# Kernel optimization log

Measured on AMD Instinct MI355X. Metric: run time of the kernel, lower is better.

## Reference

```python
import jax, jax.numpy as jnp
import numpy as np
from jax.scipy.linalg import expm

D = 512      # d_model
S = 3        # num_scales
BATCH = 256
H = 8        # attention heads
HD = D // H  # head dim


def layernorm(x, g, b, eps=1e-5):
    m = jnp.mean(x, axis=-1, keepdims=True)
    v = jnp.var(x, axis=-1, keepdims=True)
    return (x - m) / jnp.sqrt(v + eps) * g + b


def setup_inputs() -> dict:
    key = jax.random.key(0)
    ks = jax.random.split(key, 16)
    sd = 1.0 / np.sqrt(D)
    inp = {
        'x': jax.random.normal(ks[0], (BATCH, D), jnp.float32),
        'h_prev': jax.random.normal(ks[1], (BATCH, D), jnp.float32),
        'lstm_h': jax.random.normal(ks[2], (S, BATCH, D), jnp.float32) * 0.1,
        'lstm_c': jax.random.normal(ks[3], (S, BATCH, D), jnp.float32) * 0.1,
        'A': jax.random.normal(ks[4], (D, D), jnp.float32) * sd,
        'Bm': jax.random.normal(ks[5], (D, D), jnp.float32) * sd,
        'dn_w1': jax.random.normal(ks[6], (D, D), jnp.float32) * sd,
        'dn_b1': jnp.zeros((D,), jnp.float32),
        'dn_g': jnp.ones((D,), jnp.float32),
        'dn_beta': jnp.zeros((D,), jnp.float32),
        'dn_w2': jax.random.normal(ks[7], (1, D), jnp.float32) * sd,
        'dn_b2': jnp.zeros((1,), jnp.float32),
        'lstm_wih': jax.random.normal(ks[8], (S, 4 * D, D), jnp.float32) * sd,
        'lstm_whh': jax.random.normal(ks[9], (S, 4 * D, D), jnp.float32) * sd,
        'lstm_bih': jnp.zeros((S, 4 * D), jnp.float32),
        'lstm_bhh': jnp.zeros((S, 4 * D), jnp.float32),
        'decays': jnp.linspace(0.5, 0.95, S, dtype=jnp.float32),
        'attn_in_w': jax.random.normal(ks[10], (3 * D, D), jnp.float32) * sd,
        'attn_in_b': jnp.zeros((3 * D,), jnp.float32),
        'attn_out_w': jax.random.normal(ks[11], (D, D), jnp.float32) * sd,
        'attn_out_b': jnp.zeros((D,), jnp.float32),
        'proj_w': jax.random.normal(ks[12], (D, (S + 2) * D), jnp.float32) * (1.0 / np.sqrt((S + 2) * D)),
        'proj_b': jnp.zeros((D,), jnp.float32),
        'proj_g': jnp.ones((D,), jnp.float32),
        'proj_beta': jnp.zeros((D,), jnp.float32),
    }
    return inp


def reference(x, h_prev, lstm_h, lstm_c, A, Bm, dn_w1, dn_b1, dn_g, dn_beta,
              dn_w2, dn_b2, lstm_wih, lstm_whh, lstm_bih, lstm_bhh, decays,
              attn_in_w, attn_in_b, attn_out_w, attn_out_b,
              proj_w, proj_b, proj_g, proj_beta):
    # ---- delta_net: Linear -> LayerNorm -> GELU(exact) -> Linear -> Softplus ----
    h1 = layernorm(x @ dn_w1.T + dn_b1, dn_g, dn_beta)
    h1 = jax.nn.gelu(h1, approximate=False)
    delta = jax.nn.softplus(h1 @ dn_w2.T + dn_b2)           # (B, 1)

    # ---- SSM update: h_t = expm(delta*A) h_prev + delta*B x ----
    A_disc = jax.vmap(expm)(delta[:, :, None] * A)          # (B, D, D)
    h_ssm = jnp.einsum('bij,bj->bi', A_disc, h_prev) + delta * jnp.einsum('ij,bj->bi', Bm, x)

    # ---- multi-scale LSTM cells (vectorized over scales) ----
    gates = (jnp.einsum('bd,skd->sbk', x, lstm_wih)
             + jnp.einsum('sbd,skd->sbk', lstm_h, lstm_whh)
             + (lstm_bih + lstm_bhh)[:, None, :])           # (S, B, 4D)
    gi, gf, gg, go = jnp.split(gates, 4, axis=-1)
    i_g = jax.nn.sigmoid(gi)
    f_g = jax.nn.sigmoid(gf)
    g_g = jnp.tanh(gg)
    o_g = jax.nn.sigmoid(go)
    c_raw = f_g * lstm_c + i_g * g_g                        # (S, B, D)
    h_new = o_g * jnp.tanh(c_raw)                           # (S, B, D)
    dec = decays[:, None, None]
    c_new = dec * lstm_c + (1.0 - dec) * c_raw              # (S, B, D)

    # ---- fusion attention: 1 query (h_ssm), S keys/values (h_new) ----
    Wq, Wk, Wv = jnp.split(attn_in_w, 3, axis=0)
    bq, bk, bv = jnp.split(attn_in_b, 3, axis=0)
    kv = jnp.transpose(h_new, (1, 0, 2))                    # (B, S, D)
    q = (h_ssm @ Wq.T + bq).reshape(-1, 1, H, HD).transpose(0, 2, 1, 3)   # (B,H,1,HD)
    k = (kv @ Wk.T + bk).reshape(-1, S, H, HD).transpose(0, 2, 1, 3)      # (B,H,S,HD)
    v = (kv @ Wv.T + bv).reshape(-1, S, H, HD).transpose(0, 2, 1, 3)
    scores = jnp.einsum('bhqe,bhke->bhqk', q, k) / np.sqrt(HD)
    attn = jax.nn.softmax(scores, axis=-1)
    ctx = jnp.einsum('bhqk,bhke->bhqe', attn, v)            # (B,H,1,HD)
    ctx = ctx.transpose(0, 2, 1, 3).reshape(-1, D)          # (B, D)
    fused = ctx @ attn_out_w.T + attn_out_b                 # (B, D)

    # ---- output projection over concat [h_ssm, fused, h_1..h_S] ----
    combined = jnp.concatenate([h_ssm, fused] + [h_new[i] for i in range(S)], axis=-1)
    output = layernorm(combined @ proj_w.T + proj_b, proj_g, proj_beta)
    return (output, h_ssm, h_new, c_new)
```

## Files before the change

kernel.cpp:

```cpp
#include <hip/hip_runtime.h>
#include <math.h>

#define DIM 512
#define NB 256
#define KMAX 12

using bf16x8 = __attribute__((ext_vector_type(8))) short;
using f32x4  = __attribute__((ext_vector_type(4))) float;
using float4v = __attribute__((ext_vector_type(4))) float;
using ushort4v = __attribute__((ext_vector_type(4))) unsigned short;

__device__ __forceinline__ unsigned short f2b(float f) {
    union { float f; unsigned int u; } v; v.f = f;
    unsigned int r = v.u + 0x7fffu + ((v.u >> 16) & 1u);
    return (unsigned short)(r >> 16);
}
__device__ __forceinline__ float b2f(unsigned short u) {
    union { unsigned int u; float f; } v; v.u = ((unsigned int)u) << 16;
    return v.f;
}
__device__ __forceinline__ ushort4v f2b4(float4v v) {
    ushort4v o;
    o.x = f2b(v.x); o.y = f2b(v.y); o.z = f2b(v.z); o.w = f2b(v.w);
    return o;
}

__device__ __forceinline__ void block_reduce2(float& s, float& q, float* sb1, float* sb2)
{
    int tid = threadIdx.x;
    #pragma unroll
    for (int off = 32; off > 0; off >>= 1) {
        s += __shfl_down(s, off);
        q += __shfl_down(q, off);
    }
    if ((tid & 63) == 0) { sb1[tid >> 6] = s; sb2[tid >> 6] = q; }
    __syncthreads();
    s = sb1[0] + sb1[1] + sb1[2] + sb1[3];
    q = sb2[0] + sb2[1] + sb2[2] + sb2[3];
    __syncthreads();
}

struct GemmDesc {
    const unsigned short* X;
    const unsigned short* W;
    const float* bias;
    float* Cf;
    unsigned short* Cb;
    unsigned short* Ct;
    int M, N, K, ldX, ldW, ldC, tr_row0, acc, xf32, wf32;
};
struct GemmArgs { GemmDesc d[10]; };
struct LnParams {
    const float* pre; const float* g; const float* beta;
    const float* w2; const float* b2; float* delta; float* coeff;
    int lnd_y;
};
struct PwParams {
    const float* gates; const float* bih; const float* bhh; const float* cin;
    const float* decays; float* hout; float* cout; unsigned short* combb;
    int pw_y;
};

__device__ __forceinline__ void stage_op(const unsigned short* Xp, int ld, int f32flag,
    int row, int schk, int kt, unsigned short* lptr, int bufi)
{
    if (f32flag) {
        const float* Xf = (const float*)Xp;
        const float* src = Xf + (size_t)row * ld + kt * 128 + schk * 8;
        #pragma unroll
        for (int hh = 0; hh < 4; ++hh) {
            float4v v0 = *(const float4v*)(src + hh * 32);
            float4v v1 = *(const float4v*)(src + hh * 32 + 4);
            unsigned short* d = lptr + bufi * 8192 + hh * 2048;
            *(ushort4v*)d       = f2b4(v0);
            *(ushort4v*)(d + 4) = f2b4(v1);
        }
    } else {
        const unsigned short* g = Xp + (size_t)row * ld + schk * 8;
        #pragma unroll
        for (int hh = 0; hh < 4; ++hh)
            __builtin_amdgcn_global_load_lds(
                (const __attribute__((address_space(1))) unsigned int*)(g + (size_t)kt * 128 + hh * 32),
                (__attribute__((address_space(3))) unsigned int*)(lptr + bufi * 8192 + hh * 2048), 16, 0, 0);
    }
}

__global__ __launch_bounds__(256) void gemm_mfma(GemmArgs args, LnParams lp, PwParams pp)
{
    __shared__ unsigned short lsA[2][8192];
    __shared__ unsigned short lsB[2][8192];
    __shared__ float sb1[4], sb2[4];

    if ((int)blockIdx.y == lp.lnd_y) {
        int b = blockIdx.x, tid = threadIdx.x;
        if (b >= 256) return;
        int i0 = tid, i1 = tid + 256;
        float x0 = lp.pre[(size_t)b * DIM + i0];
        float x1 = lp.pre[(size_t)b * DIM + i1];
        float s = x0 + x1, q = x0 * x0 + x1 * x1;
        block_reduce2(s, q, sb1, sb2);
        float mean = s * (1.f / DIM);
        float var  = q * (1.f / DIM) - mean * mean;
        float inv  = rsqrtf(var + 1e-5f);
        float y0 = (x0 - mean) * inv * lp.g[i0] + lp.beta[i0];
        float y1 = (x1 - mean) * inv * lp.g[i1] + lp.beta[i1];
        float h0 = 0.5f * y0 * (1.f + erff(y0 * 0.70710678118654752f));
        float h1 = 0.5f * y1 * (1.f + erff(y1 * 0.70710678118654752f));
        float p = h0 * lp.w2[i0] + h1 * lp.w2[i1];
        float dummy = 0.f;
        block_reduce2(p, dummy, sb1, sb2);
        if (tid == 0) {
            float z = p + lp.b2[0];
            float d = (z > 20.f) ? z : log1pf(expf(z));
            lp.delta[b] = d;
            float c = 1.f;
            lp.coeff[b] = 1.f;
            for (int k = 1; k <= KMAX; ++k) { c *= d / (float)k; lp.coeff[k * 256 + b] = c; }
        }
        return;
    }
    if ((int)blockIdx.y == pp.pw_y) {
        int idx4 = blockIdx.x * 256 + threadIdx.x;
        if (idx4 >= 98304) return;
        int i2 = idx4 * 4;
        int s = i2 / (NB * DIM);
        int r = i2 - s * (NB * DIM);
        int b = r >> 9, d = r & 511;
        const float* gr = pp.gates + (size_t)s * 524288 + (size_t)b * 2048 + d;
        const float* bi = pp.bih + s * 2048 + d;
        const float* bh = pp.bhh + s * 2048 + d;
        float4v gi = *(const float4v*)(gr);
        float4v gf = *(const float4v*)(gr + 512);
        float4v gg = *(const float4v*)(gr + 1024);
        float4v go = *(const float4v*)(gr + 1536);
        float4v bi0 = *(const float4v*)(bi),        bh0 = *(const float4v*)(bh);
        float4v bi1 = *(const float4v*)(bi + 512),  bh1 = *(const float4v*)(bh + 512);
        float4v bi2 = *(const float4v*)(bi + 1024), bh2 = *(const float4v*)(bh + 1024);
        float4v bi3 = *(const float4v*)(bi + 1536), bh3 = *(const float4v*)(bh + 1536);
        float4v c = *(const float4v*)(pp.cin + i2);
        float dec = pp.decays[s];
        float4v hn, cn;
        #pragma unroll
        for (int j = 0; j < 4; ++j) {
            float vgi = ((const float*)&gi)[j] + ((const float*)&bi0)[j] + ((const float*)&bh0)[j];
            float vgf = ((const float*)&gf)[j] + ((const float*)&bi1)[j] + ((const float*)&bh1)[j];
            float vgg = ((const float*)&gg)[j] + ((const float*)&bi2)[j] + ((const float*)&bh2)[j];
            float vgo = ((const float*)&go)[j] + ((const float*)&bi3)[j] + ((const float*)&bh3)[j];
            float ig = 1.f / (1.f + expf(-vgi));
            float fg = 1.f / (1.f + expf(-vgf));
            float g_ = tanhf(vgg);
            float og = 1.f / (1.f + expf(-vgo));
            float cc = ((const float*)&c)[j];
            float craw = fg * cc + ig * g_;
            ((float*)&hn)[j] = og * tanhf(craw);
            ((float*)&cn)[j] = dec * cc + (1.f - dec) * craw;
        }
        *(float4v*)(pp.hout + i2) = hn;
        *(float4v*)(pp.cout + i2) = cn;
        *(ushort4v*)(pp.combb + (size_t)b * 2048 + 512 + s * 512 + d) = f2b4(hn);
        return;
    }

    GemmDesc de = args.d[blockIdx.y];
    int tn = de.N >> 6;
    int tiles = (de.M >> 6) * tn;
    int t = blockIdx.x;
    if (t >= tiles) return;
    int m0 = (t / tn) << 6;
    int n0 = (t % tn) << 6;

    int tid = threadIdx.x;
    int w = tid >> 6;
    int l = tid & 63;
    int nkt = de.K >> 7;

    int srow = w * 16 + (l >> 2);
    int schk = l & 3;
    unsigned short* lA = &lsA[0][(w * 64 + l) * 8];
    unsigned short* lB = &lsB[0][(w * 64 + l) * 8];

    int mbase = (w >> 1) * 32;
    int nbase = (w & 1) * 32;

    f32x4 acc[2][2];
    #pragma unroll
    for (int i = 0; i < 2; ++i)
        #pragma unroll
        for (int j = 0; j < 2; ++j)
            acc[i][j] = (f32x4){0.f, 0.f, 0.f, 0.f};

    int kg = l >> 4;
    int fr = l & 15;
    int aslot = (mbase * 4 + fr * 4 + kg) * 8;
    int bslot = (nbase * 4 + fr * 4 + kg) * 8;

    stage_op(de.X, de.ldX, de.xf32, m0 + srow, schk, 0, lA, 0);
    stage_op(de.W, de.ldW, de.wf32, n0 + srow, schk, 0, lB, 0);

    for (int kt = 0; kt < nkt; ++kt) {
        __syncthreads();
        if (kt + 1 < nkt) {
            stage_op(de.X, de.ldX, de.xf32, m0 + srow, schk, kt + 1, lA, (kt + 1) & 1);
            stage_op(de.W, de.ldW, de.wf32, n0 + srow, schk, kt + 1, lB, (kt + 1) & 1);
        }
        const unsigned short* bufA = &lsA[kt & 1][0];
        const unsigned short* bufB = &lsB[kt & 1][0];
        #pragma unroll
        for (int h = 0; h < 4; ++h) {
            bf16x8 a0 = *(const bf16x8*)(bufA + h * 2048 + aslot);
            bf16x8 a1 = *(const bf16x8*)(bufA + h * 2048 + aslot + 512);
            bf16x8 b0 = *(const bf16x8*)(bufB + h * 2048 + bslot);
            bf16x8 b1 = *(const bf16x8*)(bufB + h * 2048 + bslot + 512);
            acc[0][0] = __builtin_amdgcn_mfma_f32_16x16x32_bf16(a0, b0, acc[0][0], 0, 0, 0);
            acc[0][1] = __builtin_amdgcn_mfma_f32_16x16x32_bf16(a0, b1, acc[0][1], 0, 0, 0);
            acc[1][0] = __builtin_amdgcn_mfma_f32_16x16x32_bf16(a1, b0, acc[1][0], 0, 0, 0);
            acc[1][1] = __builtin_amdgcn_mfma_f32_16x16x32_bf16(a1, b1, acc[1][1], 0, 0, 0);
        }
        __syncthreads();
    }

    #pragma unroll
    for (int mi = 0; mi < 2; ++mi) {
        #pragma unroll
        for (int ni = 0; ni < 2; ++ni) {
            int col = n0 + nbase + ni * 16 + fr;
            float bv = de.bias ? de.bias[col] : 0.f;
            #pragma unroll
            for (int r = 0; r < 4; ++r) {
                int row = m0 + mbase + mi * 16 + (l >> 4) * 4 + r;
                float v = acc[mi][ni][r] + bv;
                if (de.Cf) {
                    if (de.acc == 2)      atomicAdd(&de.Cf[(size_t)row * de.ldC + col], v);
                    else if (de.acc == 1) de.Cf[(size_t)row * de.ldC + col] += v;
                    else                  de.Cf[(size_t)row * de.ldC + col] = v;
                } else {
                    de.Cb[(size_t)row * de.ldC + col] = f2b(v);
                }
                if (de.Ct && row >= de.tr_row0)
                    de.Ct[(size_t)col * 512 + (row - de.tr_row0)] = f2b(v);
            }
        }
    }
}

__global__ __launch_bounds__(256) void prep0(
    const float* __restrict__ A, unsigned short* __restrict__ ATb,
    float* __restrict__ gates, const float* __restrict__ proj_b,
    float* __restrict__ projout)
{
    __shared__ float tile[32][33];
    int bid = blockIdx.x, tid = threadIdx.x;
    if (bid < 256) {
        int bx = bid & 15, by = bid >> 4;
        int tx = tid & 31, ty = tid >> 5;
        #pragma unroll
        for (int i = 0; i < 32; i += 8)
            tile[ty + i][tx] = A[(size_t)(by * 32 + ty + i) * 512 + bx * 32 + tx];
        __syncthreads();
        #pragma unroll
        for (int i = 0; i < 32; i += 8)
            ATb[(size_t)(bx * 32 + ty + i) * 512 + by * 32 + tx] = f2b(tile[tx][ty + i]);
    } else {
        const int gstride = 128 * 256;
        int g0 = (bid - 256) * 256 + tid;
        float4v z = (float4v){0.f, 0.f, 0.f, 0.f};
        for (int i = g0; i < 393216; i += gstride)
            ((float4v*)gates)[i] = z;
        for (int i = g0; i < 32768; i += gstride) {
            float4v pb = *(const float4v*)(proj_b + (i & 127) * 4);
            ((float4v*)projout)[i] = pb;
        }
    }
}

__global__ __launch_bounds__(256) void pwh_kernel(
    const float* __restrict__ Tm, const float* __restrict__ coeff,
    const float* __restrict__ h_prev, const float* __restrict__ delta,
    const float* __restrict__ Bx, float* __restrict__ hssm,
    unsigned short* __restrict__ combb)
{
    int idx4 = blockIdx.x * 256 + threadIdx.x;
    int base = idx4 * 4;
    int b = base >> 9, i = base & 511;
    const float* Tr = Tm + (size_t)b * (KMAX * DIM) + i;
    float4v a = *(const float4v*)(h_prev + base);
    #pragma unroll
    for (int k = 1; k <= KMAX; ++k) {
        float c = coeff[k * 256 + b];
        float4v t = *(const float4v*)(Tr + (size_t)(k - 1) * DIM);
        a.x += c * t.x; a.y += c * t.y; a.z += c * t.z; a.w += c * t.w;
    }
    float dl = delta[b];
    float4v bx = *(const float4v*)(Bx + base);
    a.x += dl * bx.x; a.y += dl * bx.y; a.z += dl * bx.z; a.w += dl * bx.w;
    *(float4v*)(hssm + base) = a;
    *(ushort4v*)(combb + (size_t)b * 2048 + i) = f2b4(a);
}

__global__ __launch_bounds__(256) void tail_kernel(
    const unsigned short* __restrict__ qb, const unsigned short* __restrict__ kvb,
    const float* __restrict__ aout_w, const float* __restrict__ aout_b,
    const float* __restrict__ proj_w, const float* __restrict__ projA,
    const float* __restrict__ fin_g, const float* __restrict__ fin_beta,
    float* __restrict__ outp)
{
    __shared__ float ctxs[512];
    __shared__ float fusedl[512];
    __shared__ float totals[512];
    __shared__ float sb1[4], sb2[4];
    int b = blockIdx.x, tid = threadIdx.x;

    if (tid < 128) {
        int h = tid >> 4, sub = (tid & 15) * 4;
        int col = h * 64 + sub;
        ushort4v q4 = *(const ushort4v*)(qb + (size_t)b * 512 + col);
        float qf[4] = { b2f(q4.x), b2f(q4.y), b2f(q4.z), b2f(q4.w) };
        float p[3];
        ushort4v k4[3], v4[3];
        #pragma unroll
        for (int s = 0; s < 3; ++s) {
            k4[s] = *(const ushort4v*)(kvb + (size_t)s * 262144 + (size_t)b * 1024 + col);
            v4[s] = *(const ushort4v*)(kvb + (size_t)s * 262144 + (size_t)b * 1024 + 512 + col);
            p[s] = qf[0] * b2f(k4[s].x) + qf[1] * b2f(k4[s].y)
                 + qf[2] * b2f(k4[s].z) + qf[3] * b2f(k4[s].w);
        }
        #pragma unroll
        for (int off = 1; off < 16; off <<= 1) {
            p[0] += __shfl_xor(p[0], off);
            p[1] += __shfl_xor(p[1], off);
            p[2] += __shfl_xor(p[2], off);
        }
        const float scale = 0.125f;
        float p0 = p[0] * scale, p1 = p[1] * scale, p2 = p[2] * scale;
        float m = fmaxf(p0, fmaxf(p1, p2));
        float w0 = expf(p0 - m), w1 = expf(p1 - m), w2 = expf(p2 - m);
        float invs = 1.f / (w0 + w1 + w2);
        ctxs[col + 0] = (w0 * b2f(v4[0].x) + w1 * b2f(v4[1].x) + w2 * b2f(v4[2].x)) * invs;
        ctxs[col + 1] = (w0 * b2f(v4[0].y) + w1 * b2f(v4[1].y) + w2 * b2f(v4[2].y)) * invs;
        ctxs[col + 2] = (w0 * b2f(v4[0].z) + w1 * b2f(v4[1].z) + w2 * b2f(v4[2].z)) * invs;
        ctxs[col + 3] = (w0 * b2f(v4[0].w) + w1 * b2f(v4[1].w) + w2 * b2f(v4[2].w)) * invs;
    }
    __syncthreads();

    for (int jj = tid; jj < 512; jj += 256) {
        float acc = aout_b[jj];
        const float* wr = aout_w + (size_t)jj * 512;
        for (int k = 0; k < 512; k += 8) {
            float4v w0 = *(const float4v*)(wr + k);
            float4v w1 = *(const float4v*)(wr + k + 4);
            acc += ctxs[k+0]*w0.x + ctxs[k+1]*w0.y + ctxs[k+2]*w0.z + ctxs[k+3]*w0.w
                 + ctxs[k+4]*w1.x + ctxs[k+5]*w1.y + ctxs[k+6]*w1.z + ctxs[k+7]*w1.w;
        }
        fusedl[jj] = acc;
    }
    __syncthreads();

    for (int ii = tid; ii < 512; ii += 256) {
        float acc = projA[(size_t)b * 512 + ii];
        const float* pr = proj_w + (size_t)ii * 2560 + 512;
        for (int j = 0; j < 512; j += 8) {
            float4v w0 = *(const float4v*)(pr + j);
            float4v w1 = *(const float4v*)(pr + j + 4);
            acc += fusedl[j+0]*w0.x + fusedl[j+1]*w0.y + fusedl[j+2]*w0.z + fusedl[j+3]*w0.w
                 + fusedl[j+4]*w1.x + fusedl[j+5]*w1.y + fusedl[j+6]*w1.z + fusedl[j+7]*w1.w;
        }
        totals[ii] = acc;
    }
    __syncthreads();

    float x0 = totals[tid], x1 = totals[tid + 256];
    float s = x0 + x1, q = x0 * x0 + x1 * x1;
    block_reduce2(s, q, sb1, sb2);
    float mean = s * (1.f / DIM);
    float var  = q * (1.f / DIM) - mean * mean;
    float inv  = rsqrtf(var + 1e-5f);
    outp[(size_t)b * DIM + tid]       = (x0 - mean) * inv * fin_g[tid]       + fin_beta[tid];
    outp[(size_t)b * DIM + tid + 256] = (x1 - mean) * inv * fin_g[tid + 256] + fin_beta[tid + 256];
}

extern "C" void kernel_launch(void* const* d_in, const int* in_sizes, int n_in,
                              void* d_out, int out_size, void* d_ws, size_t ws_size,
                              hipStream_t stream)
{
    const float* x        = (const float*)d_in[0];
    const float* h_prev   = (const float*)d_in[1];
    const float* lstm_h   = (const float*)d_in[2];
    const float* lstm_c   = (const float*)d_in[3];
    const float* A        = (const float*)d_in[4];
    const float* Bm       = (const float*)d_in[5];
    const float* dn_w1    = (const float*)d_in[6];
    const float* dn_b1    = (const float*)d_in[7];
    const float* dn_g     = (const float*)d_in[8];
    const float* dn_beta  = (const float*)d_in[9];
    const float* dn_w2    = (const float*)d_in[10];
    const float* dn_b2    = (const float*)d_in[11];
    const float* wih      = (const float*)d_in[12];
    const float* whh      = (const float*)d_in[13];
    const float* bih      = (const float*)d_in[14];
    const float* bhh      = (const float*)d_in[15];
    const float* decays   = (const float*)d_in[16];
    const float* ain_w    = (const float*)d_in[17];
    const float* ain_b    = (const float*)d_in[18];
    const float* aout_w   = (const float*)d_in[19];
    const float* aout_b   = (const float*)d_in[20];
    const float* proj_w   = (const float*)d_in[21];
    const float* proj_b   = (const float*)d_in[22];
    const float* proj_g   = (const float*)d_in[23];
    const float* proj_bt  = (const float*)d_in[24];

    float* out  = (float*)d_out;
    float* hssm = out + 131072;
    float* hnew = out + 262144;
    float* cnew = out + 655360;

    unsigned short* us = (unsigned short*)d_ws;
    unsigned short* ATb   = us;
    unsigned short* P     = us + 262144;
    unsigned short* Qa    = us + 2097152;
    unsigned short* Qb    = us + 2359296;
    unsigned short* combb = us + 2621440;
    unsigned short* qb    = us + 3145728;
    unsigned short* kvb   = us + 3276800;
    unsigned short* U8b   = us + 4063232;
    float* fbase  = (float*)(us + 4194304);
    float* pre1    = fbase;
    float* delta   = fbase + 131072;
    float* coeff   = fbase + 131328;
    float* Bx      = fbase + 134656;
    float* Tm      = fbase + 265728;
    float* gates   = fbase + 1838592;
    float* projout = fbase + 3411456;

    LnParams lpOff; lpOff.pre=nullptr; lpOff.g=nullptr; lpOff.beta=nullptr;
    lpOff.w2=nullptr; lpOff.b2=nullptr; lpOff.delta=nullptr; lpOff.coeff=nullptr; lpOff.lnd_y=-1;
    PwParams ppOff; ppOff.gates=nullptr; ppOff.bih=nullptr; ppOff.bhh=nullptr; ppOff.cin=nullptr;
    ppOff.decays=nullptr; ppOff.hout=nullptr; ppOff.cout=nullptr; ppOff.combb=nullptr; ppOff.pw_y=-1;

    #define US(p) ((const unsigned short*)(p))

    prep0<<<384, 256, 0, stream>>>(A, ATb, gates, proj_b, projout);

    GemmArgs ga;
    GemmDesc z0 = { nullptr,nullptr,nullptr,nullptr,nullptr,nullptr, 0,64,128,0,0,0,0,0,0,0 };
    for (int i = 0; i < 10; ++i) ga.d[i] = z0;

    ga.d[0] = { US(x), US(dn_w1), dn_b1, pre1, nullptr, nullptr, 256,512,512, 512,512,512, 0,0, 1,1 };
    ga.d[1] = { US(x), US(Bm),   nullptr, Bx,  nullptr, nullptr, 256,512,512, 512,512,512, 0,0, 1,1 };
    ga.d[2] = { US(A), ATb,      nullptr, nullptr, P, Qa,        512,512,512, 512,512,512, 0,0, 1,0 };
    for (int s = 0; s < 3; ++s) {
        ga.d[3+s*2]   = { US(x), US(wih + (size_t)s*1048576), nullptr, gates + (size_t)s*524288,
                          nullptr, nullptr, 256,2048,512, 512,512,2048, 0,2, 1,1 };
        ga.d[4+s*2]   = { US(lstm_h + (size_t)s*131072), US(whh + (size_t)s*1048576), nullptr,
                          gates + (size_t)s*524288, nullptr, nullptr, 256,2048,512, 512,512,2048, 0,2, 1,1 };
    }
    gemm_mfma<<<dim3(128, 9), 256, 0, stream>>>(ga, lpOff, ppOff);

    for (int i = 0; i < 10; ++i) ga.d[i] = z0;
    ga.d[0] = { US(A), Qa, nullptr, nullptr, P + 1*262144, nullptr, 512,512,512, 512,512,512, 0,0, 1,0 };
    ga.d[1] = { P,     Qa, nullptr, nullptr, P + 2*262144, Qb,      512,512,512, 512,512,512, 0,0, 0,0 };
    LnParams lp1 = { pre1, dn_g, dn_beta, dn_w2, dn_b2, delta, coeff, 2 };
    PwParams pp1 = { gates, bih, bhh, lstm_c, decays, hnew, cnew, combb, 3 };
    gemm_mfma<<<dim3(384, 4), 256, 0, stream>>>(ga, lp1, pp1);

    for (int i = 0; i < 10; ++i) ga.d[i] = z0;
    ga.d[0] = { US(A), Qb, nullptr, nullptr, P + 3*262144, nullptr, 512,512,512, 512,512,512, 0,0, 1,0 };
    ga.d[1] = { P,     Qb, nullptr, nullptr, P + 4*262144, nullptr, 1536,512,512, 512,512,512, 0,0, 0,0 };
    ga.d[2] = { US(h_prev), US(A), nullptr, Tm,       nullptr, nullptr, 256,512,512,  512,512,6144, 0,0, 1,1 };
    ga.d[3] = { US(h_prev), P,     nullptr, Tm + 512, nullptr, nullptr, 256,1536,512, 512,512,6144, 0,0, 1,0 };
    for (int s = 0; s < 3; ++s) {
        ga.d[4+s] = { combb + 512 + (size_t)s*512, US(ain_w + 262144), ain_b + 512,
                      nullptr, kvb + (size_t)s*262144, nullptr, 256,1024,512, 2048,512,1024, 0,0, 0,1 };
        ga.d[7+s] = { combb + 512 + (size_t)s*512, US(proj_w + 1024 + (size_t)s*512), nullptr,
                      projout, nullptr, nullptr, 256,512,512, 2048,2560,512, 0,2, 0,1 };
    }
    gemm_mfma<<<dim3(192, 10), 256, 0, stream>>>(ga, lpOff, ppOff);

    for (int i = 0; i < 10; ++i) ga.d[i] = z0;
    ga.d[0] = { US(h_prev), P + 3*262144, nullptr, Tm + 4*512, nullptr, nullptr, 256,2048,512, 512,512,6144, 0,0, 1,0 };
    ga.d[1] = { US(h_prev), P + 6*262144, nullptr, nullptr, U8b, nullptr, 256,512,512, 512,512,512, 0,0, 1,0 };
    gemm_mfma<<<dim3(128, 2), 256, 0, stream>>>(ga, lpOff, ppOff);

    for (int i = 0; i < 10; ++i) ga.d[i] = z0;
    ga.d[0] = { U8b, US(A), nullptr, Tm + 8*512, nullptr, nullptr, 256,512,512,  512,512,6144, 0,0, 0,1 };
    ga.d[1] = { U8b, P,     nullptr, Tm + 9*512, nullptr, nullptr, 256,1536,512, 512,512,6144, 0,0, 0,0 };
    gemm_mfma<<<dim3(96, 2), 256, 0, stream>>>(ga, lpOff, ppOff);

    pwh_kernel<<<128, 256, 0, stream>>>(Tm, coeff, h_prev, delta, Bx, hssm, combb);

    for (int i = 0; i < 10; ++i) ga.d[i] = z0;
    ga.d[0] = { combb, US(ain_w),  ain_b,  nullptr, qb, nullptr, 256,512,512, 2048,512,512, 0,0, 0,1 };
    ga.d[1] = { combb, US(proj_w), nullptr, projout, nullptr, nullptr, 256,512,512, 2048,2560,512, 0,2, 0,1 };
    gemm_mfma<<<dim3(32, 2), 256, 0, stream>>>(ga, lpOff, ppOff);

    tail_kernel<<<256, 256, 0, stream>>>(qb, kvb, aout_w, aout_b, proj_w, projout,
                                         proj_g, proj_bt, out);
    #undef US
}
```

Measured before the change: 266.8 us.

## Fuse h_ssm combine with q/proj GEMV and use bf16 weights in tail

Merges the pwh elementwise kernel and the small MFMA GEMM that computed q and the h_ssm part of the projection into one per-batch-row kernel. It keeps h_ssm in shared memory and does two GEMVs over bf16 copies of Wq and proj_w's first block. Weight conversions to bf16 (attn_out_w, Wq, two proj_w slices) are added to prep0, and tail_kernel reads the bf16 copies to halve weight traffic. This drops one launch and one gemm dependency. The cost is scalar GEMV work in place of MFMA for the q/proj part, and the same weight rows are read by all 256 blocks.

```diff
diff --git a/kernel.cpp b/kernel.cpp
--- a/kernel.cpp
+++ b/kernel.cpp
@@ -246,7 +246,11 @@
 __global__ __launch_bounds__(256) void prep0(
     const float* __restrict__ A, unsigned short* __restrict__ ATb,
     float* __restrict__ gates, const float* __restrict__ proj_b,
-    float* __restrict__ projout)
+    float* __restrict__ projout,
+    const float* __restrict__ aout_w, unsigned short* __restrict__ aout_wb,
+    const float* __restrict__ ain_w,  unsigned short* __restrict__ Wqb,
+    const float* __restrict__ proj_w, unsigned short* __restrict__ P0b,
+    unsigned short* __restrict__ P2b)
 {
     __shared__ float tile[32][33];
     int bid = blockIdx.x, tid = threadIdx.x;
@@ -260,7 +264,7 @@
         #pragma unroll
         for (int i = 0; i < 32; i += 8)
             ATb[(size_t)(bx * 32 + ty + i) * 512 + by * 32 + tx] = f2b(tile[tx][ty + i]);
-    } else {
+    } else if (bid < 384) {
         const int gstride = 128 * 256;
         int g0 = (bid - 256) * 256 + tid;
         float4v z = (float4v){0.f, 0.f, 0.f, 0.f};
@@ -270,37 +274,70 @@
             float4v pb = *(const float4v*)(proj_b + (i & 127) * 4);
             ((float4v*)projout)[i] = pb;
         }
-    }
-}
-
-__global__ __launch_bounds__(256) void pwh_kernel(
+    } else {
+        const int gstride = 256 * 256;
+        int g0 = (bid - 384) * 256 + tid;
+        for (int i = g0; i < 65536; i += gstride) {
+            *(ushort4v*)(aout_wb + (size_t)i * 4) = f2b4(((const float4v*)aout_w)[i]);
+            *(ushort4v*)(Wqb + (size_t)i * 4)     = f2b4(((const float4v*)ain_w)[i]);
+            int row = i >> 7, c = i & 127;
+            *(ushort4v*)(P0b + (size_t)i * 4) =
+                f2b4(*(const float4v*)(proj_w + (size_t)row * 2560 + c * 4));
+            *(ushort4v*)(P2b + (size_t)i * 4) =
+                f2b4(*(const float4v*)(proj_w + (size_t)row * 2560 + 512 + c * 4));
+        }
+    }
+}
+
+__global__ __launch_bounds__(256) void pwh2_kernel(
     const float* __restrict__ Tm, const float* __restrict__ coeff,
     const float* __restrict__ h_prev, const float* __restrict__ delta,
     const float* __restrict__ Bx, float* __restrict__ hssm,
-    unsigned short* __restrict__ combb)
-{
-    int idx4 = blockIdx.x * 256 + threadIdx.x;
-    int base = idx4 * 4;
-    int b = base >> 9, i = base & 511;
-    const float* Tr = Tm + (size_t)b * (KMAX * DIM) + i;
-    float4v a = *(const float4v*)(h_prev + base);
-    #pragma unroll
-    for (int k = 1; k <= KMAX; ++k) {
-        float c = coeff[k * 256 + b];
-        float4v t = *(const float4v*)(Tr + (size_t)(k - 1) * DIM);
-        a.x += c * t.x; a.y += c * t.y; a.z += c * t.z; a.w += c * t.w;
-    }
+    unsigned short* __restrict__ combb,
+    const unsigned short* __restrict__ Wqb, const float* __restrict__ ain_b,
+    const unsigned short* __restrict__ P0b,
+    unsigned short* __restrict__ qb, float* __restrict__ projout)
+{
+    __shared__ float hs[512];
+    int b = blockIdx.x, tid = threadIdx.x;
     float dl = delta[b];
-    float4v bx = *(const float4v*)(Bx + base);
-    a.x += dl * bx.x; a.y += dl * bx.y; a.z += dl * bx.z; a.w += dl * bx.w;
-    *(float4v*)(hssm + base) = a;
-    *(ushort4v*)(combb + (size_t)b * 2048 + i) = f2b4(a);
+    for (int ii = tid; ii < 512; ii += 256) {
+        const float* Tr = Tm + (size_t)b * (KMAX * DIM) + ii;
+        float a = h_prev[(size_t)b * 512 + ii];
+        #pragma unroll
+        for (int k = 1; k <= KMAX; ++k)
+            a += coeff[k * 256 + b] * Tr[(size_t)(k - 1) * DIM];
+        a += dl * Bx[(size_t)b * 512 + ii];
+        hs[ii] = a;
+        hssm[(size_t)b * 512 + ii] = a;
+        combb[(size_t)b * 2048 + ii] = f2b(a);
+    }
+    __syncthreads();
+
+    for (int jj = tid; jj < 512; jj += 256) {
+        float aq = ain_b[jj];
+        float ap = projout[(size_t)b * 512 + jj];
+        const unsigned short* wq = Wqb + (size_t)jj * 512;
+        const unsigned short* p0 = P0b + (size_t)jj * 512;
+        for (int k = 0; k < 512; k += 8) {
+            ushort4v q0 = *(const ushort4v*)(wq + k);
+            ushort4v q1 = *(const ushort4v*)(wq + k + 4);
+            ushort4v r0 = *(const ushort4v*)(p0 + k);
+            ushort4v r1 = *(const ushort4v*)(p0 + k + 4);
+            aq += hs[k+0]*b2f(q0.x) + hs[k+1]*b2f(q0.y) + hs[k+2]*b2f(q0.z) + hs[k+3]*b2f(q0.w)
+                + hs[k+4]*b2f(q1.x) + hs[k+5]*b2f(q1.y) + hs[k+6]*b2f(q1.z) + hs[k+7]*b2f(q1.w);
+            ap += hs[k+0]*b2f(r0.x) + hs[k+1]*b2f(r0.y) + hs[k+2]*b2f(r0.z) + hs[k+3]*b2f(r0.w)
+                + hs[k+4]*b2f(r1.x) + hs[k+5]*b2f(r1.y) + hs[k+6]*b2f(r1.z) + hs[k+7]*b2f(r1.w);
+        }
+        qb[(size_t)b * 512 + jj] = f2b(aq);
+        projout[(size_t)b * 512 + jj] = ap;
+    }
 }
 
 __global__ __launch_bounds__(256) void tail_kernel(
     const unsigned short* __restrict__ qb, const unsigned short* __restrict__ kvb,
-    const float* __restrict__ aout_w, const float* __restrict__ aout_b,
-    const float* __restrict__ proj_w, const float* __restrict__ projA,
+    const unsigned short* __restrict__ aout_wb, const float* __restrict__ aout_b,
+    const unsigned short* __restrict__ P2b, const float* __restrict__ projA,
     const float* __restrict__ fin_g, const float* __restrict__ fin_beta,
     float* __restrict__ outp)
 {
@@ -344,12 +381,14 @@
 
     for (int jj = tid; jj < 512; jj += 256) {
         float acc = aout_b[jj];
-        const float* wr = aout_w + (size_t)jj * 512;
+        const unsigned short* wr = aout_wb + (size_t)jj * 512;
         for (int k = 0; k < 512; k += 8) {
-            float4v w0 = *(const float4v*)(wr + k);
-            float4v w1 = *(const float4v*)(wr + k + 4);
-            acc += ctxs[k+0]*w0.x + ctxs[k+1]*w0.y + ctxs[k+2]*w0.z + ctxs[k+3]*w0.w
-                 + ctxs[k+4]*w1.x + ctxs[k+5]*w1.y + ctxs[k+6]*w1.z + ctxs[k+7]*w1.w;
+            ushort4v w0 = *(const ushort4v*)(wr + k);
+            ushort4v w1 = *(const ushort4v*)(wr + k + 4);
+            acc += ctxs[k+0]*b2f(w0.x) + ctxs[k+1]*b2f(w0.y)
+                 + ctxs[k+2]*b2f(w0.z) + ctxs[k+3]*b2f(w0.w)
+                 + ctxs[k+4]*b2f(w1.x) + ctxs[k+5]*b2f(w1.y)
+                 + ctxs[k+6]*b2f(w1.z) + ctxs[k+7]*b2f(w1.w);
         }
         fusedl[jj] = acc;
     }
@@ -357,12 +396,14 @@
 
     for (int ii = tid; ii < 512; ii += 256) {
         float acc = projA[(size_t)b * 512 + ii];
-        const float* pr = proj_w + (size_t)ii * 2560 + 512;
+        const unsigned short* pr = P2b + (size_t)ii * 512;
         for (int j = 0; j < 512; j += 8) {
-            float4v w0 = *(const float4v*)(pr + j);
-            float4v w1 = *(const float4v*)(pr + j + 4);
-            acc += fusedl[j+0]*w0.x + fusedl[j+1]*w0.y + fusedl[j+2]*w0.z + fusedl[j+3]*w0.w
-                 + fusedl[j+4]*w1.x + fusedl[j+5]*w1.y + fusedl[j+6]*w1.z + fusedl[j+7]*w1.w;
+            ushort4v w0 = *(const ushort4v*)(pr + j);
+            ushort4v w1 = *(const ushort4v*)(pr + j + 4);
+            acc += fusedl[j+0]*b2f(w0.x) + fusedl[j+1]*b2f(w0.y)
+                 + fusedl[j+2]*b2f(w0.z) + fusedl[j+3]*b2f(w0.w)
+                 + fusedl[j+4]*b2f(w1.x) + fusedl[j+5]*b2f(w1.y)
+                 + fusedl[j+6]*b2f(w1.z) + fusedl[j+7]*b2f(w1.w);
         }
         totals[ii] = acc;
     }
@@ -414,15 +455,19 @@
     float* cnew = out + 655360;
 
     unsigned short* us = (unsigned short*)d_ws;
-    unsigned short* ATb   = us;
-    unsigned short* P     = us + 262144;
-    unsigned short* Qa    = us + 2097152;
-    unsigned short* Qb    = us + 2359296;
-    unsigned short* combb = us + 2621440;
-    unsigned short* qb    = us + 3145728;
-    unsigned short* kvb   = us + 3276800;
-    unsigned short* U8b   = us + 4063232;
-    float* fbase  = (float*)(us + 4194304);
+    unsigned short* ATb     = us;
+    unsigned short* P       = us + 262144;
+    unsigned short* Qa      = us + 2097152;
+    unsigned short* Qb      = us + 2359296;
+    unsigned short* combb   = us + 2621440;
+    unsigned short* qb      = us + 3145728;
+    unsigned short* kvb     = us + 3276800;
+    unsigned short* U8b     = us + 4063232;
+    unsigned short* aout_wb = us + 4194304;
+    unsigned short* Wqb     = us + 4456448;
+    unsigned short* P0b     = us + 4718592;
+    unsigned short* P2b     = us + 4980736;
+    float* fbase  = (float*)(us + 5242880);
     float* pre1    = fbase;
     float* delta   = fbase + 131072;
     float* coeff   = fbase + 131328;
@@ -438,7 +483,8 @@
 
     #define US(p) ((const unsigned short*)(p))
 
-    prep0<<<384, 256, 0, stream>>>(A, ATb, gates, proj_b, projout);
+    prep0<<<640, 256, 0, stream>>>(A, ATb, gates, proj_b, projout,
+                                   aout_w, aout_wb, ain_w, Wqb, proj_w, P0b, P2b);
 
     GemmArgs ga;
     GemmDesc z0 = { nullptr,nullptr,nullptr,nullptr,nullptr,nullptr, 0,64,128,0,0,0,0,0,0,0 };
@@ -448,10 +494,10 @@
     ga.d[1] = { US(x), US(Bm),   nullptr, Bx,  nullptr, nullptr, 256,512,512, 512,512,512, 0,0, 1,1 };
     ga.d[2] = { US(A), ATb,      nullptr, nullptr, P, Qa,        512,512,512, 512,512,512, 0,0, 1,0 };
     for (int s = 0; s < 3; ++s) {
-        ga.d[3+s*2]   = { US(x), US(wih + (size_t)s*1048576), nullptr, gates + (size_t)s*524288,
-                          nullptr, nullptr, 256,2048,512, 512,512,2048, 0,2, 1,1 };
-        ga.d[4+s*2]   = { US(lstm_h + (size_t)s*131072), US(whh + (size_t)s*1048576), nullptr,
-                          gates + (size_t)s*524288, nullptr, nullptr, 256,2048,512, 512,512,2048, 0,2, 1,1 };
+        ga.d[3+s*2] = { US(x), US(wih + (size_t)s*1048576), nullptr, gates + (size_t)s*524288,
+                        nullptr, nullptr, 256,2048,512, 512,512,2048, 0,2, 1,1 };
+        ga.d[4+s*2] = { US(lstm_h + (size_t)s*131072), US(whh + (size_t)s*1048576), nullptr,
+                        gates + (size_t)s*524288, nullptr, nullptr, 256,2048,512, 512,512,2048, 0,2, 1,1 };
     }
     gemm_mfma<<<dim3(128, 9), 256, 0, stream>>>(ga, lpOff, ppOff);
 
@@ -485,14 +531,10 @@
     ga.d[1] = { U8b, P,     nullptr, Tm + 9*512, nullptr, nullptr, 256,1536,512, 512,512,6144, 0,0, 0,0 };
     gemm_mfma<<<dim3(96, 2), 256, 0, stream>>>(ga, lpOff, ppOff);
 
-    pwh_kernel<<<128, 256, 0, stream>>>(Tm, coeff, h_prev, delta, Bx, hssm, combb);
-
-    for (int i = 0; i < 10; ++i) ga.d[i] = z0;
-    ga.d[0] = { combb, US(ain_w),  ain_b,  nullptr, qb, nullptr, 256,512,512, 2048,512,512, 0,0, 0,1 };
-    ga.d[1] = { combb, US(proj_w), nullptr, projout, nullptr, nullptr, 256,512,512, 2048,2560,512, 0,2, 0,1 };
-    gemm_mfma<<<dim3(32, 2), 256, 0, stream>>>(ga, lpOff, ppOff);
-
-    tail_kernel<<<256, 256, 0, stream>>>(qb, kvb, aout_w, aout_b, proj_w, projout,
+    pwh2_kernel<<<256, 256, 0, stream>>>(Tm, coeff, h_prev, delta, Bx, hssm, combb,
+                                         Wqb, ain_b, P0b, qb, projout);
+
+    tail_kernel<<<256, 256, 0, stream>>>(qb, kvb, aout_wb, aout_b, P2b, projout,
                                          proj_g, proj_bt, out);
     #undef US
 }
```

Measured after the change: 264.2 us. No clear change (-1.0%).
